# Optimization experiments

Measured on AMD Instinct MI355X. Metric: run time of the kernel, lower is better.

Reference implementation:

```python
import jax, jax.numpy as jnp
import numpy as np

E, H, M = 1024, 16, 256
B, S = 2, 2048
D = E // H
SCALE = D ** -0.5


def setup_inputs() -> dict:
    key = jax.random.key(0)
    ks = jax.random.split(key, 10)
    p = 0.02
    return {
        "x": jax.random.normal(ks[0], (B, S, E), jnp.float32),
        "Wq": jax.random.normal(ks[1], (E, E), jnp.float32) * p,
        "bq": jax.random.normal(ks[2], (E,), jnp.float32) * p,
        "Wk": jax.random.normal(ks[3], (E, E), jnp.float32) * p,
        "bk": jax.random.normal(ks[4], (E,), jnp.float32) * p,
        "Wv": jax.random.normal(ks[5], (E, E), jnp.float32) * p,
        "bv": jax.random.normal(ks[6], (E,), jnp.float32) * p,
        "Wo": jax.random.normal(ks[7], (E, E), jnp.float32) * p,
        "bo": jax.random.normal(ks[8], (E,), jnp.float32) * p,
        "memory_state": jax.random.normal(ks[9], (M, E), jnp.float32) * p,
    }


def reference(x, Wq, bq, Wk, bk, Wv, bv, Wo, bo, memory_state):
    b, s, e = x.shape
    # QKV projections (torch Linear: y = x W^T + b), split heads -> [b,h,s,d]
    q = (x @ Wq.T + bq).reshape(b, s, H, D).transpose(0, 2, 1, 3)
    k = (x @ Wk.T + bk).reshape(b, s, H, D).transpose(0, 2, 1, 3)
    v = (x @ Wv.T + bv).reshape(b, s, H, D).transpose(0, 2, 1, 3)
    # full self-attention (eval mode: dropout is identity)
    attn = jax.nn.softmax(jnp.einsum("bhqd,bhkd->bhqk", q, k) * SCALE, axis=-1)
    attn_out = jnp.einsum("bhqk,bhkd->bhqd", attn, v)
    attn_out = attn_out.transpose(0, 2, 1, 3).reshape(b, s, e)
    # memory-read cross-attention on raw x against compressed memory [M,E]
    mem_w = jax.nn.softmax(jnp.einsum("bse,me->bsm", x, memory_state) * SCALE, axis=-1)
    mem_out = jnp.einsum("bsm,me->bse", mem_w, memory_state)
    out = attn_out + 0.5 * mem_out
    return out @ Wo.T + bo
```

## Files before the change

### kernel.cpp

```cpp
#include <hip/hip_runtime.h>
#include <cstdint>
#include <cstddef>


typedef __bf16 bf16;
typedef bf16  bf16x8 __attribute__((ext_vector_type(8)));
typedef bf16  bf16x4 __attribute__((ext_vector_type(4)));
typedef float f32x4  __attribute__((ext_vector_type(4)));
typedef float f32x16 __attribute__((ext_vector_type(16)));
typedef int   i32x4  __attribute__((ext_vector_type(4)));
typedef int   i32x2  __attribute__((ext_vector_type(2)));

#define B_DIM 2
#define S_DIM 2048
#define E_DIM 1024
#define H_DIM 16
#define D_DIM 64
#define M_DIM 256
#define NROW  (B_DIM * S_DIM)
#define C1 0.18033688011112042f

#define MFMA32(a, b, c) __builtin_amdgcn_mfma_f32_32x32x16_bf16((a), (b), (c), 0, 0, 0)

__device__ __forceinline__ f32x16 zero16()
{
    f32x16 z;
#pragma unroll
    for (int i = 0; i < 16; ++i) z[i] = 0.f;
    return z;
}

__device__ __forceinline__ void async_cp16(const bf16* g, bf16* l)
{
    __builtin_amdgcn_global_load_lds(
        (const __attribute__((address_space(1))) void*)g,
        (__attribute__((address_space(3))) void*)l, 16, 0, 0);
}

__global__ void __launch_bounds__(256)
conv_all(const float* __restrict__ x,  const float* __restrict__ Wq,
         const float* __restrict__ Wk, const float* __restrict__ Wv,
         const float* __restrict__ Wo, const float* __restrict__ mem,
         bf16* __restrict__ xb,  bf16* __restrict__ Wqb,
         bf16* __restrict__ Wkb, bf16* __restrict__ Wvb,
         bf16* __restrict__ Wob, bf16* __restrict__ memb,
         bf16* __restrict__ memt)
{
    int t = blockIdx.x * 256 + threadIdx.x;
    const float* src; bf16* dst; int off; bool is_mem = false;
    if      (t <  524288) { src = x;   dst = xb;   off = t; }
    else if (t <  655360) { src = Wq;  dst = Wqb;  off = t - 524288; }
    else if (t <  786432) { src = Wk;  dst = Wkb;  off = t - 655360; }
    else if (t <  917504) { src = Wv;  dst = Wvb;  off = t - 786432; }
    else if (t < 1048576) { src = Wo;  dst = Wob;  off = t - 917504; }
    else                  { src = mem; dst = memb; off = t - 1048576; is_mem = true; }
    const float4* p = (const float4*)src + (size_t)off * 2;
    float4 a = p[0], b = p[1];
    bf16x8 o;
    o[0] = (bf16)a.x; o[1] = (bf16)a.y; o[2] = (bf16)a.z; o[3] = (bf16)a.w;
    o[4] = (bf16)b.x; o[5] = (bf16)b.y; o[6] = (bf16)b.z; o[7] = (bf16)b.w;
    *(bf16x8*)(dst + (size_t)off * 8) = o;
    if (is_mem) {
        int r = off >> 7, c0 = (off & 127) * 8;
        float h[8] = {a.x, a.y, a.z, a.w, b.x, b.y, b.z, b.w};
#pragma unroll
        for (int j = 0; j < 8; ++j)
            memt[(size_t)(c0 + j) * M_DIM + r] = (bf16)(0.5f * h[j]);
    }
}

struct GemmAcc { f32x4 a[4][4]; };

__device__ __forceinline__ void
gemm_core(const bf16* __restrict__ A, const bf16* __restrict__ Bm,
          int K, int m0, int n0, bf16* As, bf16* Bs, GemmAcc& R)
{
    const int tid  = threadIdx.x;
    const int lane = tid & 63;
    const int wave = tid >> 6;
    const int quad = lane >> 4;
    const int l16  = lane & 15;
    const int wm   = (wave >> 1) * 64;
    const int wn   = (wave & 1) * 64;

#pragma unroll
    for (int i = 0; i < 4; ++i)
#pragma unroll
        for (int j = 0; j < 4; ++j)
            R.a[i][j] = f32x4{0.f, 0.f, 0.f, 0.f};

    int s_c0  = wave * 128 + lane;
    int s_r0  = s_c0 >> 2;
    int s_k0  = (s_c0 & 3) ^ ((s_r0 >> 1) & 3);
    int s_c1  = s_c0 + 64;
    int s_r1  = s_c1 >> 2;
    int s_k1  = (s_c1 & 3) ^ ((s_r1 >> 1) & 3);
    const bf16* gA0 = A  + (size_t)(m0 + s_r0) * K + s_k0 * 8;
    const bf16* gA1 = A  + (size_t)(m0 + s_r1) * K + s_k1 * 8;
    const bf16* gB0 = Bm + (size_t)(n0 + s_r0) * K + s_k0 * 8;
    const bf16* gB1 = Bm + (size_t)(n0 + s_r1) * K + s_k1 * 8;

#define STAGE(buf, k0)                                                     \
    do {                                                                   \
        async_cp16(gA0 + (k0), &As[(buf) * 4096 + wave * 1024]);           \
        async_cp16(gA1 + (k0), &As[(buf) * 4096 + wave * 1024 + 512]);     \
        async_cp16(gB0 + (k0), &Bs[(buf) * 4096 + wave * 1024]);           \
        async_cp16(gB1 + (k0), &Bs[(buf) * 4096 + wave * 1024 + 512]);     \
    } while (0)

    STAGE(0, 0);
    int buf = 0;
    for (int k0 = 0; k0 < K; k0 += 32) {
        __syncthreads();
        if (k0 + 32 < K) STAGE(buf ^ 1, k0 + 32);

        const bf16* Ab = As + buf * 4096;
        const bf16* Bb = Bs + buf * 4096;
        bf16x8 af[4], bfr[4];
#pragma unroll
        for (int mi = 0; mi < 4; ++mi) {
            int m    = wm + mi * 16 + l16;
            int slot = quad ^ ((m >> 1) & 3);
            af[mi]   = *(const bf16x8*)(&Ab[(m * 4 + slot) * 8]);
        }
#pragma unroll
        for (int ni = 0; ni < 4; ++ni) {
            int n    = wn + ni * 16 + l16;
            int slot = quad ^ ((n >> 1) & 3);
            bfr[ni]  = *(const bf16x8*)(&Bb[(n * 4 + slot) * 8]);
        }
#pragma unroll
        for (int mi = 0; mi < 4; ++mi)
#pragma unroll
            for (int ni = 0; ni < 4; ++ni)
                R.a[mi][ni] = __builtin_amdgcn_mfma_f32_16x16x32_bf16(
                    af[mi], bfr[ni], R.a[mi][ni], 0, 0, 0);
        buf ^= 1;
    }
#undef STAGE
}

__global__ void __launch_bounds__(256, 3)
gemm_qkvl(const bf16* __restrict__ A,
          const bf16* __restrict__ Wq, const bf16* __restrict__ Wk,
          const bf16* __restrict__ Wv, const bf16* __restrict__ memb,
          const float* __restrict__ bq, const float* __restrict__ bk,
          const float* __restrict__ bv,
          bf16* __restrict__ q, bf16* __restrict__ k,
          bf16* __restrict__ vt, bf16* __restrict__ lg)
{
    __shared__ __align__(16) bf16 As[2 * 4096];
    __shared__ __align__(16) bf16 Bs[2 * 4096];
    const int lid  = blockIdx.x;
    const int xcd  = lid & 7;
    const int idx  = lid >> 3;
    const int mloc = idx / 26;
    const int nn   = idx - mloc * 26;
    const int m0   = (mloc * 8 + xcd) * 128;
    const int widx = (nn < 24) ? (nn >> 3) : 3;
    const int n0   = (nn < 24) ? (nn & 7) * 128 : (nn - 24) * 128;
    const bf16*  Bm = (widx == 0) ? Wq : (widx == 1) ? Wk :
                      (widx == 2) ? Wv : memb;
    GemmAcc R;
    gemm_core(A, Bm, E_DIM, m0, n0, As, Bs, R);

    const int lane = threadIdx.x & 63, wave = threadIdx.x >> 6;
    const int quad = lane >> 4, l16 = lane & 15;
    const int wm = (wave >> 1) * 64, wn = (wave & 1) * 64;

    if (widx == 0 || widx == 1) {
        bf16* C = (widx == 0) ? q : k;
        const float* bi = (widx == 0) ? bq : bk;
        float scale = (widx == 0) ? C1 : 1.0f;
#pragma unroll
        for (int ni = 0; ni < 4; ++ni) {
            int col  = n0 + wn + ni * 16 + l16;
            float bb = bi[col];
#pragma unroll
            for (int mi = 0; mi < 4; ++mi)
#pragma unroll
                for (int r = 0; r < 4; ++r) {
                    int rowg = m0 + wm + mi * 16 + quad * 4 + r;
                    C[(size_t)rowg * E_DIM + col] =
                        (bf16)((R.a[mi][ni][r] + bb) * scale);
                }
        }
    } else if (widx == 2) {
#pragma unroll
        for (int ni = 0; ni < 4; ++ni) {
            int col = n0 + wn + ni * 16 + l16;
            float bb = bv[col];
#pragma unroll
            for (int mi = 0; mi < 4; ++mi) {
                int row0 = m0 + wm + mi * 16 + quad * 4;
                int bidx = row0 >> 11, s = row0 & 2047;
                bf16x4 pk;
#pragma unroll
                for (int r = 0; r < 4; ++r) pk[r] = (bf16)(R.a[mi][ni][r] + bb);
                *(bf16x4*)(&vt[((size_t)(bidx * H_DIM) * 64 + col) * S_DIM + s]) = pk;
            }
        }
    } else {
#pragma unroll
        for (int ni = 0; ni < 4; ++ni) {
            int col = n0 + wn + ni * 16 + l16;
#pragma unroll
            for (int mi = 0; mi < 4; ++mi)
#pragma unroll
                for (int r = 0; r < 4; ++r) {
                    int rowg = m0 + wm + mi * 16 + quad * 4 + r;
                    lg[(size_t)rowg * M_DIM + col] = (bf16)R.a[mi][ni][r];
                }
        }
    }
}

__global__ void __launch_bounds__(256, 2)
gemm_out64(const bf16* __restrict__ A, const bf16* __restrict__ Bm,
           const float* __restrict__ bias, float* __restrict__ C)
{
    __shared__ __align__(16) bf16 As[2 * 2048];
    __shared__ __align__(16) bf16 Bs[2 * 4096];
    const int tid  = threadIdx.x;
    const int lane = tid & 63;
    const int wave = tid >> 6;
    const int quad = lane >> 4;
    const int l16  = lane & 15;
    const int wm   = (wave >> 1) * 32;
    const int wn   = (wave & 1) * 64;
    const int lid  = blockIdx.x;
    const int xcd  = lid & 7;
    const int idx  = lid >> 3;
    const int mloc = idx >> 3;
    const int nn   = idx & 7;
    const int m0   = (mloc * 8 + xcd) * 64;
    const int n0   = nn * 128;
    const int K    = E_DIM;

    f32x4 acc[2][4];
#pragma unroll
    for (int i = 0; i < 2; ++i)
#pragma unroll
        for (int j = 0; j < 4; ++j) acc[i][j] = f32x4{0.f, 0.f, 0.f, 0.f};

    int a_s  = wave * 64 + lane;
    int a_r  = a_s >> 2;
    int a_k  = (a_s & 3) ^ ((a_r >> 1) & 3);
    int b_s0 = wave * 128 + lane;
    int b_r0 = b_s0 >> 2;
    int b_k0 = (b_s0 & 3) ^ ((b_r0 >> 1) & 3);
    int b_s1 = b_s0 + 64;
    int b_r1 = b_s1 >> 2;
    int b_k1 = (b_s1 & 3) ^ ((b_r1 >> 1) & 3);
    const bf16* gA  = A  + (size_t)(m0 + a_r) * K + a_k * 8;
    const bf16* gB0 = Bm + (size_t)(n0 + b_r0) * K + b_k0 * 8;
    const bf16* gB1 = Bm + (size_t)(n0 + b_r1) * K + b_k1 * 8;

#define STAGE64(buf, k0)                                                   \
    do {                                                                   \
        async_cp16(gA  + (k0), &As[(buf) * 2048 + wave * 512]);            \
        async_cp16(gB0 + (k0), &Bs[(buf) * 4096 + wave * 1024]);           \
        async_cp16(gB1 + (k0), &Bs[(buf) * 4096 + wave * 1024 + 512]);     \
    } while (0)

    STAGE64(0, 0);
    int buf = 0;
    for (int k0 = 0; k0 < K; k0 += 32) {
        __syncthreads();
        if (k0 + 32 < K) STAGE64(buf ^ 1, k0 + 32);
        const bf16* Ab = As + buf * 2048;
        const bf16* Bb = Bs + buf * 4096;
        bf16x8 af[2], bfr[4];
#pragma unroll
        for (int mi = 0; mi < 2; ++mi) {
            int m    = wm + mi * 16 + l16;
            int slot = quad ^ ((m >> 1) & 3);
            af[mi]   = *(const bf16x8*)(&Ab[(m * 4 + slot) * 8]);
        }
#pragma unroll
        for (int ni = 0; ni < 4; ++ni) {
            int n    = wn + ni * 16 + l16;
            int slot = quad ^ ((n >> 1) & 3);
            bfr[ni]  = *(const bf16x8*)(&Bb[(n * 4 + slot) * 8]);
        }
#pragma unroll
        for (int mi = 0; mi < 2; ++mi)
#pragma unroll
            for (int ni = 0; ni < 4; ++ni)
                acc[mi][ni] = __builtin_amdgcn_mfma_f32_16x16x32_bf16(
                    af[mi], bfr[ni], acc[mi][ni], 0, 0, 0);
        buf ^= 1;
    }
#undef STAGE64

#pragma unroll
    for (int ni = 0; ni < 4; ++ni) {
        int col  = n0 + wn + ni * 16 + l16;
        float bb = bias[col];
#pragma unroll
        for (int mi = 0; mi < 2; ++mi)
#pragma unroll
            for (int r = 0; r < 4; ++r) {
                int rowg = m0 + wm + mi * 16 + quad * 4 + r;
                C[(size_t)rowg * E_DIM + col] = acc[mi][ni][r] + bb;
            }
    }
}

__global__ void __launch_bounds__(256, 2)
flash_attn(const bf16* __restrict__ q, const bf16* __restrict__ k,
           const bf16* __restrict__ vt, const bf16* __restrict__ lg,
           const bf16* __restrict__ memt, bf16* __restrict__ outc)
{
    __shared__ __align__(16) bf16 Ks[2 * 4096];
    __shared__ __align__(16) bf16 Vs[2 * 4096];
    const int tid  = threadIdx.x;
    const int lane = tid & 63;
    const int wave = tid >> 6;
    const int hi   = lane >> 5;
    const int l32  = lane & 31;
    const int lid = blockIdx.x;
    const int xcd = lid & 7;
    const int kk  = lid >> 3;
    const int qt  = kk & 15;
    const int p   = ((kk >> 4) << 3) | xcd;
    const int b   = p >> 4;
    const int h   = p & 15;
    const int q0  = qt * 128 + wave * 32;

    const bf16* qb = q  + (size_t)(b * S_DIM + q0) * E_DIM + h * D_DIM;
    const bf16* kb = k  + (size_t)(b * S_DIM) * E_DIM + h * D_DIM;
    const bf16* vb = vt + (size_t)(b * H_DIM + h) * D_DIM * S_DIM;

    const int s_s0 = wave * 128 + lane;
    const int s_r0 = s_s0 >> 3;
    const int s_g0 = (s_s0 & 7) ^ (s_r0 & 7);
    const int s_s1 = s_s0 + 64;
    const int s_r1 = s_s1 >> 3;
    const int s_g1 = (s_s1 & 7) ^ (s_r1 & 7);
    const bf16* gK0 = kb + (size_t)s_r0 * E_DIM + s_g0 * 8;
    const bf16* gK1 = kb + (size_t)s_r1 * E_DIM + s_g1 * 8;
    const bf16* gV0 = vb + (size_t)s_r0 * S_DIM + s_g0 * 8;
    const bf16* gV1 = vb + (size_t)s_r1 * S_DIM + s_g1 * 8;

    const int kd0 = wave * 1024 + lane * 8;
    const int v00 = s_r0 * 64 + (((s_g0 & ~1)    ) ^ (s_r0 & 7)) * 8 + (s_g0 & 1) * 4;
    const int v01 = s_r0 * 64 + (((s_g0 & ~1) | 1) ^ (s_r0 & 7)) * 8 + (s_g0 & 1) * 4;
    const int v10 = s_r1 * 64 + (((s_g1 & ~1)    ) ^ (s_r1 & 7)) * 8 + (s_g1 & 1) * 4;
    const int v11 = s_r1 * 64 + (((s_g1 & ~1) | 1) ^ (s_r1 & 7)) * 8 + (s_g1 & 1) * 4;

    bf16x8 qfr[4];
#pragma unroll
    for (int c = 0; c < 4; ++c)
        qfr[c] = *(const bf16x8*)(qb + (size_t)l32 * E_DIM + c * 16 + hi * 8);

    bf16x8 vones;
#pragma unroll
    for (int j = 0; j < 8; ++j) vones[j] = (bf16)1.0f;

    f32x16 o_acc0 = zero16(), o_acc1 = zero16(), osum = zero16();

    {
        i32x4 rK0 = *(const i32x4*)(gK0);
        i32x4 rK1 = *(const i32x4*)(gK1);
        i32x4 rV0 = *(const i32x4*)(gV0);
        i32x4 rV1 = *(const i32x4*)(gV1);
        *(i32x4*)(&Ks[kd0])       = rK0;
        *(i32x4*)(&Ks[kd0 + 512]) = rK1;
        *(i32x2*)(&Vs[v00]) = i32x2{rV0[0], rV0[1]};
        *(i32x2*)(&Vs[v01]) = i32x2{rV0[2], rV0[3]};
        *(i32x2*)(&Vs[v10]) = i32x2{rV1[0], rV1[1]};
        *(i32x2*)(&Vs[v11]) = i32x2{rV1[2], rV1[3]};
    }
    __syncthreads();

    int buf = 0;
    for (int kt = 0; kt < S_DIM; kt += 64) {
        const bool pre = (kt + 64 < S_DIM);
        i32x4 nK0, nK1, nV0, nV1;
        if (pre) {
            const size_t ko = (size_t)(kt + 64) * E_DIM;
            nK0 = *(const i32x4*)(gK0 + ko);
            nK1 = *(const i32x4*)(gK1 + ko);
            nV0 = *(const i32x4*)(gV0 + (kt + 64));
            nV1 = *(const i32x4*)(gV1 + (kt + 64));
        }
        const bf16* Kb = Ks + buf * 4096;
        const bf16* Vb = Vs + buf * 4096;

        f32x16 sc0 = zero16(), sc1 = zero16();
        __builtin_amdgcn_s_setprio(1);
#pragma unroll
        for (int c = 0; c < 4; ++c) {
            const int cc  = c * 2 + hi;
            const int swz = (cc ^ (l32 & 7)) * 8;
            bf16x8 kf0 = *(const bf16x8*)(&Kb[l32 * 64 + swz]);
            bf16x8 kf1 = *(const bf16x8*)(&Kb[(32 + l32) * 64 + swz]);
            sc0 = MFMA32(kf0, qfr[c], sc0);
            sc1 = MFMA32(kf1, qfr[c], sc1);
        }
        __builtin_amdgcn_s_setprio(0);

        bf16x8 ap[4];
#pragma unroll
        for (int kc = 0; kc < 4; ++kc) {
            const f32x16 sct = (kc < 2) ? sc0 : sc1;
            const int base = (kc & 1) * 8;
#pragma unroll
            for (int j = 0; j < 8; ++j)
                ap[kc][j] = (bf16)exp2f(sct[base + j]);
        }

        __builtin_amdgcn_s_setprio(1);
#pragma unroll
        for (int kc = 0; kc < 4; ++kc) {
            const int swz = ((kc * 2 + hi) ^ (l32 & 7)) * 8;
            bf16x8 vf0 = *(const bf16x8*)(&Vb[l32 * 64 + swz]);
            bf16x8 vf1 = *(const bf16x8*)(&Vb[(32 + l32) * 64 + swz]);
            o_acc0 = MFMA32(ap[kc], vf0, o_acc0);
            o_acc1 = MFMA32(ap[kc], vf1, o_acc1);
            osum   = MFMA32(ap[kc], vones, osum);
        }
        __builtin_amdgcn_s_setprio(0);

        if (pre) {
            const int bo = (buf ^ 1) * 4096;
            *(i32x4*)(&Ks[bo + kd0])       = nK0;
            *(i32x4*)(&Ks[bo + kd0 + 512]) = nK1;
            *(i32x2*)(&Vs[bo + v00]) = i32x2{nV0[0], nV0[1]};
            *(i32x2*)(&Vs[bo + v01]) = i32x2{nV0[2], nV0[3]};
            *(i32x2*)(&Vs[bo + v10]) = i32x2{nV1[0], nV1[1]};
            *(i32x2*)(&Vs[bo + v11]) = i32x2{nV1[2], nV1[3]};
        }
        __syncthreads();
        buf ^= 1;
    }

    float linv[16];
#pragma unroll
    for (int r = 0; r < 16; ++r) linv[r] = 1.f / osum[r];

    const bf16* Pr = lg   + (size_t)(b * S_DIM + q0) * M_DIM;
    const bf16* Mt = memt + (size_t)(h * D_DIM) * M_DIM;
    f32x16 macc0 = zero16(), macc1 = zero16(), msum = zero16();
#pragma unroll
    for (int mc = 0; mc < 16; ++mc) {
        bf16x8 raw = *(const bf16x8*)(Pr + (size_t)l32 * M_DIM + mc * 16 + hi * 8);
        bf16x8 epv;
#pragma unroll
        for (int j = 0; j < 8; ++j) epv[j] = (bf16)exp2f(C1 * (float)raw[j]);
        bf16x8 bm0 = *(const bf16x8*)(Mt + (size_t)l32 * M_DIM        + mc * 16 + hi * 8);
        bf16x8 bm1 = *(const bf16x8*)(Mt + (size_t)(32 + l32) * M_DIM + mc * 16 + hi * 8);
        macc0 = MFMA32(epv, bm0, macc0);
        macc1 = MFMA32(epv, bm1, macc1);
        msum  = MFMA32(epv, vones, msum);
    }

    bf16* ob = outc + (size_t)(b * S_DIM + q0) * E_DIM + h * D_DIM;
#pragma unroll
    for (int r = 0; r < 16; ++r) {
        const int qrow = (r & 3) + 8 * (r >> 2) + 4 * hi;
        const float mi = 1.f / msum[r];
        ob[(size_t)qrow * E_DIM + l32]      = (bf16)(o_acc0[r] * linv[r] + macc0[r] * mi);
        ob[(size_t)qrow * E_DIM + 32 + l32] = (bf16)(o_acc1[r] * linv[r] + macc1[r] * mi);
    }
}

extern "C" void kernel_launch(void* const* d_in, const int* in_sizes, int n_in,
                              void* d_out, int out_size, void* d_ws, size_t ws_size,
                              hipStream_t stream)
{
    (void)in_sizes; (void)n_in; (void)out_size; (void)ws_size;
    const float* x   = (const float*)d_in[0];
    const float* Wq  = (const float*)d_in[1];
    const float* bq  = (const float*)d_in[2];
    const float* Wk  = (const float*)d_in[3];
    const float* bk  = (const float*)d_in[4];
    const float* Wv  = (const float*)d_in[5];
    const float* bv  = (const float*)d_in[6];
    const float* Wo  = (const float*)d_in[7];
    const float* bo  = (const float*)d_in[8];
    const float* mem = (const float*)d_in[9];
    float* out = (float*)d_out;

    bf16* w = (bf16*)d_ws;
    const size_t NE = (size_t)NROW * E_DIM;
    const size_t EE = (size_t)E_DIM * E_DIM;
    bf16* xb      = w;
    bf16* q_ws    = w + NE;
    bf16* k_ws    = w + 2 * NE;
    bf16* Wqb     = w + 3 * NE;
    bf16* Wkb     = Wqb + EE;
    bf16* Wvb     = Wkb + EE;
    bf16* Wob     = Wvb + EE;
    bf16* memb    = Wob + EE;
    bf16* lg_ws   = memb + (size_t)M_DIM * E_DIM;
    bf16* memt_ws = lg_ws + (size_t)NROW * M_DIM;
    bf16* vt_ws = (bf16*)d_out;

    dim3 blk(256);

    conv_all<<<dim3(4224), blk, 0, stream>>>(
        x, Wq, Wk, Wv, Wo, mem, xb, Wqb, Wkb, Wvb, Wob, memb, memt_ws);

    gemm_qkvl<<<dim3(832), blk, 0, stream>>>(
        xb, Wqb, Wkb, Wvb, memb, bq, bk, bv, q_ws, k_ws, vt_ws, lg_ws);

    flash_attn<<<dim3(512), blk, 0, stream>>>(
        q_ws, k_ws, vt_ws, lg_ws, memt_ws, q_ws);

    gemm_out64<<<dim3(512), blk, 0, stream>>>(
        q_ws, Wob, bo, out);
}
```

Before: 215.1 us.

## Split attention KV range across wave pairs and merge partials in shared memory

Each flash-attention block now handles 64 queries instead of 128. Its four waves form two query halves times two KV halves; each wave streams 1024 keys in 32-key tiles. Partial outputs and row sums are combined through shared memory, and one wave per pair then finishes the memory-attention tail. The grid doubles to 1024 blocks with launch bounds of 4 blocks per SM, aiming for more parallelism and occupancy, at the cost of reloading Q per block, an extra reduction and sync, and idle waves during the tail.

New measurement: 224.3 us. 1.04x slower.

```diff
diff --git a/kernel.cpp b/kernel.cpp
--- a/kernel.cpp
+++ b/kernel.cpp
@@ -307,47 +307,50 @@
     }
 }
 
-__global__ void __launch_bounds__(256, 2)
+__global__ void __launch_bounds__(256, 4)
 flash_attn(const bf16* __restrict__ q, const bf16* __restrict__ k,
            const bf16* __restrict__ vt, const bf16* __restrict__ lg,
            const bf16* __restrict__ memt, bf16* __restrict__ outc)
 {
-    __shared__ __align__(16) bf16 Ks[2 * 4096];
-    __shared__ __align__(16) bf16 Vs[2 * 4096];
+    __shared__ __align__(16) bf16 SM[16384];
     const int tid  = threadIdx.x;
     const int lane = tid & 63;
     const int wave = tid >> 6;
     const int hi   = lane >> 5;
     const int l32  = lane & 31;
+    const int pw   = wave & 1;
+    const int ks   = wave >> 1;
+
     const int lid = blockIdx.x;
     const int xcd = lid & 7;
     const int kk  = lid >> 3;
-    const int qt  = kk & 15;
-    const int p   = ((kk >> 4) << 3) | xcd;
+    const int qt  = kk & 31;
+    const int p   = ((kk >> 5) << 3) | xcd;
     const int b   = p >> 4;
     const int h   = p & 15;
-    const int q0  = qt * 128 + wave * 32;
-
-    const bf16* qb = q  + (size_t)(b * S_DIM + q0) * E_DIM + h * D_DIM;
+    const int q0  = qt * 64;
+    const int qw  = q0 + pw * 32;
+
+    const bf16* qb = q  + (size_t)(b * S_DIM + qw) * E_DIM + h * D_DIM;
     const bf16* kb = k  + (size_t)(b * S_DIM) * E_DIM + h * D_DIM;
     const bf16* vb = vt + (size_t)(b * H_DIM + h) * D_DIM * S_DIM;
-
-    const int s_s0 = wave * 128 + lane;
-    const int s_r0 = s_s0 >> 3;
-    const int s_g0 = (s_s0 & 7) ^ (s_r0 & 7);
-    const int s_s1 = s_s0 + 64;
-    const int s_r1 = s_s1 >> 3;
-    const int s_g1 = (s_s1 & 7) ^ (s_r1 & 7);
-    const bf16* gK0 = kb + (size_t)s_r0 * E_DIM + s_g0 * 8;
-    const bf16* gK1 = kb + (size_t)s_r1 * E_DIM + s_g1 * 8;
-    const bf16* gV0 = vb + (size_t)s_r0 * S_DIM + s_g0 * 8;
-    const bf16* gV1 = vb + (size_t)s_r1 * S_DIM + s_g1 * 8;
-
-    const int kd0 = wave * 1024 + lane * 8;
-    const int v00 = s_r0 * 64 + (((s_g0 & ~1)    ) ^ (s_r0 & 7)) * 8 + (s_g0 & 1) * 4;
-    const int v01 = s_r0 * 64 + (((s_g0 & ~1) | 1) ^ (s_r0 & 7)) * 8 + (s_g0 & 1) * 4;
-    const int v10 = s_r1 * 64 + (((s_g1 & ~1)    ) ^ (s_r1 & 7)) * 8 + (s_g1 & 1) * 4;
-    const int v11 = s_r1 * 64 + (((s_g1 & ~1) | 1) ^ (s_r1 & 7)) * 8 + (s_g1 & 1) * 4;
+    const int   kv0 = ks * 1024;
+
+    bf16* Kb0 = SM + ks * 8192;
+    bf16* Vb0 = SM + ks * 8192 + 4096;
+
+    const int pl = pw * 64 + lane;
+    const int kr0 = pl >> 3;
+    const int kg0 = (pl & 7) ^ (kr0 & 7);
+    const bf16* gK0 = kb + (size_t)(kv0 + kr0) * E_DIM + kg0 * 8;
+    const bf16* gK1 = gK0 + (size_t)16 * E_DIM;
+    const int kd0 = pl * 8;
+    const int vd0 = pl >> 2;
+    const int vg0 = (pl & 3) ^ (vd0 & 3);
+    const bf16* gV0 = vb + (size_t)vd0 * S_DIM + kv0 + vg0 * 8;
+    const bf16* gV1 = gV0 + (size_t)32 * S_DIM;
+    const int v00 = vd0 * 32 + (((vg0 & ~1)    ) ^ (vd0 & 3)) * 8 + (vg0 & 1) * 4;
+    const int v01 = vd0 * 32 + (((vg0 & ~1) | 1) ^ (vd0 & 3)) * 8 + (vg0 & 1) * 4;
 
     bf16x8 qfr[4];
 #pragma unroll
@@ -358,89 +361,105 @@
 #pragma unroll
     for (int j = 0; j < 8; ++j) vones[j] = (bf16)1.0f;
 
-    f32x16 o_acc0 = zero16(), o_acc1 = zero16(), osum = zero16();
+    f32x16 o0 = zero16(), o1 = zero16(), osum = zero16();
 
     {
         i32x4 rK0 = *(const i32x4*)(gK0);
         i32x4 rK1 = *(const i32x4*)(gK1);
         i32x4 rV0 = *(const i32x4*)(gV0);
         i32x4 rV1 = *(const i32x4*)(gV1);
-        *(i32x4*)(&Ks[kd0])       = rK0;
-        *(i32x4*)(&Ks[kd0 + 512]) = rK1;
-        *(i32x2*)(&Vs[v00]) = i32x2{rV0[0], rV0[1]};
-        *(i32x2*)(&Vs[v01]) = i32x2{rV0[2], rV0[3]};
-        *(i32x2*)(&Vs[v10]) = i32x2{rV1[0], rV1[1]};
-        *(i32x2*)(&Vs[v11]) = i32x2{rV1[2], rV1[3]};
+        *(i32x4*)(Kb0 + kd0)        = rK0;
+        *(i32x4*)(Kb0 + kd0 + 1024) = rK1;
+        *(i32x2*)(Vb0 + v00)        = i32x2{rV0[0], rV0[1]};
+        *(i32x2*)(Vb0 + v01)        = i32x2{rV0[2], rV0[3]};
+        *(i32x2*)(Vb0 + v00 + 1024) = i32x2{rV1[0], rV1[1]};
+        *(i32x2*)(Vb0 + v01 + 1024) = i32x2{rV1[2], rV1[3]};
     }
     __syncthreads();
 
     int buf = 0;
-    for (int kt = 0; kt < S_DIM; kt += 64) {
-        const bool pre = (kt + 64 < S_DIM);
+    for (int kt = 0; kt < 1024; kt += 32) {
+        const bool pre = (kt + 32 < 1024);
         i32x4 nK0, nK1, nV0, nV1;
         if (pre) {
-            const size_t ko = (size_t)(kt + 64) * E_DIM;
+            const size_t ko = (size_t)(kt + 32) * E_DIM;
             nK0 = *(const i32x4*)(gK0 + ko);
             nK1 = *(const i32x4*)(gK1 + ko);
-            nV0 = *(const i32x4*)(gV0 + (kt + 64));
-            nV1 = *(const i32x4*)(gV1 + (kt + 64));
-        }
-        const bf16* Kb = Ks + buf * 4096;
-        const bf16* Vb = Vs + buf * 4096;
-
-        f32x16 sc0 = zero16(), sc1 = zero16();
+            nV0 = *(const i32x4*)(gV0 + (kt + 32));
+            nV1 = *(const i32x4*)(gV1 + (kt + 32));
+        }
+        const bf16* Kb = Kb0 + buf * 2048;
+        const bf16* Vb = Vb0 + buf * 2048;
+
+        f32x16 sc0 = zero16();
         __builtin_amdgcn_s_setprio(1);
 #pragma unroll
         for (int c = 0; c < 4; ++c) {
-            const int cc  = c * 2 + hi;
-            const int swz = (cc ^ (l32 & 7)) * 8;
-            bf16x8 kf0 = *(const bf16x8*)(&Kb[l32 * 64 + swz]);
-            bf16x8 kf1 = *(const bf16x8*)(&Kb[(32 + l32) * 64 + swz]);
-            sc0 = MFMA32(kf0, qfr[c], sc0);
-            sc1 = MFMA32(kf1, qfr[c], sc1);
+            const int swz = ((c * 2 + hi) ^ (l32 & 7)) * 8;
+            bf16x8 kf = *(const bf16x8*)(&Kb[l32 * 64 + swz]);
+            sc0 = MFMA32(kf, qfr[c], sc0);
         }
         __builtin_amdgcn_s_setprio(0);
 
-        bf16x8 ap[4];
-#pragma unroll
-        for (int kc = 0; kc < 4; ++kc) {
-            const f32x16 sct = (kc < 2) ? sc0 : sc1;
-            const int base = (kc & 1) * 8;
+        bf16x8 ap[2];
+#pragma unroll
+        for (int kc = 0; kc < 2; ++kc)
 #pragma unroll
             for (int j = 0; j < 8; ++j)
-                ap[kc][j] = (bf16)exp2f(sct[base + j]);
-        }
+                ap[kc][j] = (bf16)exp2f(sc0[kc * 8 + j]);
 
         __builtin_amdgcn_s_setprio(1);
 #pragma unroll
-        for (int kc = 0; kc < 4; ++kc) {
-            const int swz = ((kc * 2 + hi) ^ (l32 & 7)) * 8;
-            bf16x8 vf0 = *(const bf16x8*)(&Vb[l32 * 64 + swz]);
-            bf16x8 vf1 = *(const bf16x8*)(&Vb[(32 + l32) * 64 + swz]);
-            o_acc0 = MFMA32(ap[kc], vf0, o_acc0);
-            o_acc1 = MFMA32(ap[kc], vf1, o_acc1);
-            osum   = MFMA32(ap[kc], vones, osum);
+        for (int kc = 0; kc < 2; ++kc) {
+            const int swz = ((kc * 2 + hi) ^ (l32 & 3)) * 8;
+            bf16x8 vf0 = *(const bf16x8*)(&Vb[l32 * 32 + swz]);
+            bf16x8 vf1 = *(const bf16x8*)(&Vb[(32 + l32) * 32 + swz]);
+            o0   = MFMA32(ap[kc], vf0, o0);
+            o1   = MFMA32(ap[kc], vf1, o1);
+            osum = MFMA32(ap[kc], vones, osum);
         }
         __builtin_amdgcn_s_setprio(0);
 
         if (pre) {
-            const int bo = (buf ^ 1) * 4096;
-            *(i32x4*)(&Ks[bo + kd0])       = nK0;
-            *(i32x4*)(&Ks[bo + kd0 + 512]) = nK1;
-            *(i32x2*)(&Vs[bo + v00]) = i32x2{nV0[0], nV0[1]};
-            *(i32x2*)(&Vs[bo + v01]) = i32x2{nV0[2], nV0[3]};
-            *(i32x2*)(&Vs[bo + v10]) = i32x2{nV1[0], nV1[1]};
-            *(i32x2*)(&Vs[bo + v11]) = i32x2{nV1[2], nV1[3]};
+            const int bo = (buf ^ 1) * 2048;
+            *(i32x4*)(Kb0 + bo + kd0)        = nK0;
+            *(i32x4*)(Kb0 + bo + kd0 + 1024) = nK1;
+            *(i32x2*)(Vb0 + bo + v00)        = i32x2{nV0[0], nV0[1]};
+            *(i32x2*)(Vb0 + bo + v01)        = i32x2{nV0[2], nV0[3]};
+            *(i32x2*)(Vb0 + bo + v00 + 1024) = i32x2{nV1[0], nV1[1]};
+            *(i32x2*)(Vb0 + bo + v01 + 1024) = i32x2{nV1[2], nV1[3]};
         }
         __syncthreads();
         buf ^= 1;
     }
 
+    float* smf = (float*)SM;
+    if (ks == 1) {
+        float* dst = smf + pw * 3072 + lane;
+#pragma unroll
+        for (int i = 0; i < 16; ++i) dst[i * 64]        = o0[i];
+#pragma unroll
+        for (int i = 0; i < 16; ++i) dst[(16 + i) * 64] = o1[i];
+#pragma unroll
+        for (int i = 0; i < 16; ++i) dst[(32 + i) * 64] = osum[i];
+    }
+    __syncthreads();
+    if (ks == 1) return;
+    {
+        const float* src = smf + pw * 3072 + lane;
+#pragma unroll
+        for (int i = 0; i < 16; ++i) o0[i]   += src[i * 64];
+#pragma unroll
+        for (int i = 0; i < 16; ++i) o1[i]   += src[(16 + i) * 64];
+#pragma unroll
+        for (int i = 0; i < 16; ++i) osum[i] += src[(32 + i) * 64];
+    }
+
     float linv[16];
 #pragma unroll
     for (int r = 0; r < 16; ++r) linv[r] = 1.f / osum[r];
 
-    const bf16* Pr = lg   + (size_t)(b * S_DIM + q0) * M_DIM;
+    const bf16* Pr = lg   + (size_t)(b * S_DIM + qw) * M_DIM;
     const bf16* Mt = memt + (size_t)(h * D_DIM) * M_DIM;
     f32x16 macc0 = zero16(), macc1 = zero16(), msum = zero16();
 #pragma unroll
@@ -456,13 +475,13 @@
         msum  = MFMA32(epv, vones, msum);
     }
 
-    bf16* ob = outc + (size_t)(b * S_DIM + q0) * E_DIM + h * D_DIM;
+    bf16* ob = outc + (size_t)(b * S_DIM + qw) * E_DIM + h * D_DIM;
 #pragma unroll
     for (int r = 0; r < 16; ++r) {
         const int qrow = (r & 3) + 8 * (r >> 2) + 4 * hi;
         const float mi = 1.f / msum[r];
-        ob[(size_t)qrow * E_DIM + l32]      = (bf16)(o_acc0[r] * linv[r] + macc0[r] * mi);
-        ob[(size_t)qrow * E_DIM + 32 + l32] = (bf16)(o_acc1[r] * linv[r] + macc1[r] * mi);
+        ob[(size_t)qrow * E_DIM + l32]      = (bf16)(o0[r] * linv[r] + macc0[r] * mi);
+        ob[(size_t)qrow * E_DIM + 32 + l32] = (bf16)(o1[r] * linv[r] + macc1[r] * mi);
     }
 }
 
@@ -506,7 +525,7 @@
     gemm_qkvl<<<dim3(832), blk, 0, stream>>>(
         xb, Wqb, Wkb, Wvb, memb, bq, bk, bv, q_ws, k_ws, vt_ws, lg_ws);
 
-    flash_attn<<<dim3(512), blk, 0, stream>>>(
+    flash_attn<<<dim3(1024), blk, 0, stream>>>(
         q_ws, k_ws, vt_ws, lg_ws, memt_ws, q_ws);
 
     gemm_out64<<<dim3(512), blk, 0, stream>>>(
```
